# Optimization experiments

Measured on AMD Instinct MI355X. Metric: run time of the kernel, lower is better.

Reference implementation:

```python
import jax, jax.numpy as jnp
import numpy as np

N_HEAD = 16
D_HEAD = 64
D_MODEL = 1024
B, T = 2, 2048


def setup_inputs() -> dict:
    key = jax.random.key(0)
    ks = jax.random.split(key, 5)
    s = 1.0 / np.sqrt(D_MODEL)
    return {
        "x": jax.random.normal(ks[0], (B, T, D_MODEL), dtype=jnp.float32),
        "wq": jax.random.normal(ks[1], (D_MODEL, D_MODEL), dtype=jnp.float32) * s,
        "wk": jax.random.normal(ks[2], (D_MODEL, D_MODEL), dtype=jnp.float32) * s,
        "wv": jax.random.normal(ks[3], (D_MODEL, D_MODEL), dtype=jnp.float32) * s,
        "wo": jax.random.normal(ks[4], (D_MODEL, D_MODEL), dtype=jnp.float32) * s,
    }


def reference(x, wq, wk, wv, wo):
    Bb, Tt, D = x.shape
    H, Dh = N_HEAD, D_HEAD
    # Linear projections (flax Linear: y = x @ kernel), split heads
    q = (x @ wq).reshape(Bb, Tt, H, Dh)
    k = (x @ wk).reshape(Bb, Tt, H, Dh)
    v = (x @ wv).reshape(Bb, Tt, H, Dh)
    scale = jnp.sqrt(jnp.asarray(Dh)).astype(x.dtype)
    scores = jnp.einsum('bthd,bshd->bhts', q, k) / scale  # [B,H,T,T]
    mask = jnp.tril(jnp.ones((Tt, Tt), dtype=jnp.bool_))
    scores = jnp.where(mask, scores, jnp.finfo(scores.dtype).min)
    attn = jax.nn.softmax(scores, axis=-1)
    out = jnp.einsum('bhts,bshd->bthd', attn, v).reshape(Bb, Tt, D)
    return out @ wo
```

## Files before the change

kernel.cpp:

```cpp
#include <hip/hip_runtime.h>
#include <math.h>

#define DEV static __device__ __forceinline__

typedef __attribute__((ext_vector_type(4))) float f32x4;
typedef __attribute__((ext_vector_type(2))) unsigned u32x2;
typedef __attribute__((ext_vector_type(8))) __bf16 bf16x8;
typedef __attribute__((ext_vector_type(8))) unsigned short u16x8;
typedef __attribute__((ext_vector_type(4))) unsigned short u16x4;

constexpr int TB = 2;
constexpr int TT = 2048;
constexpr int DM = 1024;
constexpr int NH = 16;
constexpr int DH = 64;
constexpr int MR = TB * TT;
constexpr int SQKV = 3 * DM;

DEV unsigned short f2bf(float f) {
  union { float f; unsigned u; } v; v.f = f;
  return (unsigned short)((v.u + 0x7FFFu + ((v.u >> 16) & 1u)) >> 16);
}

DEV unsigned cvtpk(float a, float b) {
  unsigned r;
  asm("v_cvt_pk_bf16_f32 %0, %1, %2" : "=v"(r) : "v"(a), "v"(b));
  return r;
}

DEV void gld16(const void* g, void* l) {
  __builtin_amdgcn_global_load_lds((const __attribute__((address_space(1))) void*)g,
                                   (__attribute__((address_space(3))) void*)l, 16, 0, 0);
}

DEV bf16x8 ldsb8(const unsigned short* p) { return *(const bf16x8*)p; }

__global__ __launch_bounds__(256) void k_prep(const float* __restrict__ x,
                                              const float* __restrict__ w0,
                                              const float* __restrict__ w1,
                                              const float* __restrict__ w2,
                                              const float* __restrict__ w3,
                                              unsigned short* __restrict__ xb,
                                              unsigned short* __restrict__ wtdst) {
  __shared__ float tile[32][33];
  const int id = blockIdx.x, tid = threadIdx.x;
  if (id < 4096) {
    const int z = id >> 10, tl = id & 1023;
    const float* w = z == 0 ? w0 : z == 1 ? w1 : z == 2 ? w2 : w3;
    unsigned short* wt = wtdst + (size_t)z * DM * DM;
    const int n0 = (tl & 31) * 32, k0 = (tl >> 5) * 32;
    const int tx = tid & 31, ty = tid >> 5;
#pragma unroll
    for (int yy = 0; yy < 32; yy += 8)
      tile[ty + yy][tx] = w[(size_t)(k0 + ty + yy) * DM + n0 + tx];
    __syncthreads();
#pragma unroll
    for (int yy = 0; yy < 32; yy += 8)
      wt[(size_t)(n0 + ty + yy) * DM + k0 + tx] = f2bf(tile[tx][ty + yy]);
  } else {
    const int i = ((id - 4096) * 256 + tid) * 8;
    f32x4 a = *(const f32x4*)(x + i);
    f32x4 b = *(const f32x4*)(x + i + 4);
    u16x8 o;
#pragma unroll
    for (int j = 0; j < 4; ++j) { o[j] = f2bf(a[j]); o[j + 4] = f2bf(b[j]); }
    *(u16x8*)(xb + i) = o;
  }
}

__global__ __launch_bounds__(512) void k_gemm_qkv(const unsigned short* __restrict__ A,
                                                  const unsigned short* __restrict__ Bt,
                                                  unsigned short* __restrict__ Qb,
                                                  float ascale,
                                                  unsigned short* __restrict__ kp,
                                                  unsigned short* __restrict__ vt) {
  constexpr int K = DM, NS = K / 32;
  __shared__ alignas(16) unsigned short As[2][128 * 32];
  __shared__ alignas(16) unsigned short Bs[2][128 * 32];
  const int tid = threadIdx.x;
  const int m0 = blockIdx.y * 128, n0 = blockIdx.x * 128;
  const int lane = tid & 63, w = tid >> 6;
  const int lr = lane & 15, lg = lane >> 4;
  const int wm = w >> 2, wn = w & 3;
  const int srow = tid >> 2, scc = (tid & 3) ^ ((srow >> 1) & 3);
  const unsigned short* Ab = A + (size_t)(m0 + srow) * K + scc * 8;
  const unsigned short* Bb = Bt + (size_t)(n0 + srow) * K + scc * 8;
  auto stage = [&](int buf, int s) {
    gld16(Ab + s * 32, (void*)(As[buf] + tid * 8));
    gld16(Bb + s * 32, (void*)(Bs[buf] + tid * 8));
  };
  f32x4 acc[4][2] = {};
  stage(0, 0);
  for (int s = 0; s < NS; ++s) {
    const int buf = s & 1;
    asm volatile("s_waitcnt vmcnt(0)" ::: "memory");
    __builtin_amdgcn_s_barrier();
    if (s + 1 < NS) stage(buf ^ 1, s + 1);
    bf16x8 af[4], bfr[2];
#pragma unroll
    for (int i = 0; i < 4; ++i) {
      const int row = wm * 64 + i * 16 + lr;
      af[i] = ldsb8(As[buf] + row * 32 + ((lg ^ ((row >> 1) & 3)) * 8));
    }
#pragma unroll
    for (int j = 0; j < 2; ++j) {
      const int row = wn * 32 + j * 16 + lr;
      bfr[j] = ldsb8(Bs[buf] + row * 32 + ((lg ^ ((row >> 1) & 3)) * 8));
    }
    __builtin_amdgcn_s_setprio(1);
#pragma unroll
    for (int i = 0; i < 4; ++i)
#pragma unroll
      for (int j = 0; j < 2; ++j)
        acc[i][j] = __builtin_amdgcn_mfma_f32_16x16x32_bf16(af[i], bfr[j], acc[i][j], 0, 0, 0);
    __builtin_amdgcn_s_setprio(0);
  }
#pragma unroll
  for (int i = 0; i < 4; ++i)
#pragma unroll
    for (int j = 0; j < 2; ++j) {
      const int row = m0 + wm * 64 + i * 16 + lg * 4;
      const int col = n0 + wn * 32 + j * 16 + lr;
      const int bb = row >> 11, sg = row & (TT - 1);
      if (col < DM) {
#pragma unroll
        for (int r = 0; r < 4; ++r)
          Qb[(size_t)(row + r) * DM + col] = f2bf(acc[i][j][r] * ascale);
      } else if (col < 2 * DM) {
        const int hh = (col - DM) >> 6, dd = (col - DM) & 63;
        unsigned short* kb = kp + (size_t)(bb * NH + hh) * 32 * 4096;
#pragma unroll
        for (int r = 0; r < 4; ++r) {
          const int s = sg + r, t = s >> 6, sl = s & 63;
          kb[t * 4096 + sl * 64 + (((dd >> 3) ^ (sl & 7)) * 8) + (dd & 7)] = f2bf(acc[i][j][r]);
        }
      } else {
        const int hh = (col - 2 * DM) >> 6, dd = (col - 2 * DM) & 63;
        const int t = sg >> 6, sl = sg & 63;
        const int g = ((sl >> 5) << 2) | ((sl >> 2) & 3);
        const int hf2 = (sl >> 4) & 1;
        const int cch = g ^ (dd & 7);
        u16x4 pk;
#pragma unroll
        for (int r = 0; r < 4; ++r) pk[r] = f2bf(acc[i][j][r]);
        *(u16x4*)(vt + (size_t)((bb * NH + hh) * 32 + t) * 4096 + dd * 64 + cch * 8 + hf2 * 4) = pk;
      }
    }
}

__global__ __launch_bounds__(512) void k_gemm_out(const unsigned short* __restrict__ A,
                                                  const unsigned short* __restrict__ Bt,
                                                  float* __restrict__ C) {
  constexpr int K = DM, N = DM, NS = K / 32;
  __shared__ alignas(16) unsigned short As[2][128 * 32];
  __shared__ alignas(16) unsigned short Bs[2][64 * 32];
  const int tid = threadIdx.x;
  const int m0 = blockIdx.y * 128, n0 = blockIdx.x * 64;
  const int lane = tid & 63, w = tid >> 6;
  const int lr = lane & 15, lg = lane >> 4;
  const int wm = w >> 1, wn = w & 1;
  const int srow = tid >> 2, scc = (tid & 3) ^ ((srow >> 1) & 3);
  const unsigned short* Ab = A + (size_t)(m0 + srow) * K + scc * 8;
  const unsigned short* Bb = (tid < 256) ? Bt + (size_t)(n0 + srow) * K + scc * 8 : nullptr;
  auto stage = [&](int buf, int s) {
    gld16(Ab + s * 32, (void*)(As[buf] + tid * 8));
    if (tid < 256) gld16(Bb + s * 32, (void*)(Bs[buf] + tid * 8));
  };
  f32x4 acc[2][2] = {};
  stage(0, 0);
  for (int s = 0; s < NS; ++s) {
    const int buf = s & 1;
    asm volatile("s_waitcnt vmcnt(0)" ::: "memory");
    __builtin_amdgcn_s_barrier();
    if (s + 1 < NS) stage(buf ^ 1, s + 1);
    bf16x8 af[2], bfr[2];
#pragma unroll
    for (int i = 0; i < 2; ++i) {
      const int row = wm * 32 + i * 16 + lr;
      af[i] = ldsb8(As[buf] + row * 32 + ((lg ^ ((row >> 1) & 3)) * 8));
    }
#pragma unroll
    for (int j = 0; j < 2; ++j) {
      const int row = wn * 32 + j * 16 + lr;
      bfr[j] = ldsb8(Bs[buf] + row * 32 + ((lg ^ ((row >> 1) & 3)) * 8));
    }
    __builtin_amdgcn_s_setprio(1);
#pragma unroll
    for (int i = 0; i < 2; ++i)
#pragma unroll
      for (int j = 0; j < 2; ++j)
        acc[i][j] = __builtin_amdgcn_mfma_f32_16x16x32_bf16(af[i], bfr[j], acc[i][j], 0, 0, 0);
    __builtin_amdgcn_s_setprio(0);
  }
#pragma unroll
  for (int i = 0; i < 2; ++i)
#pragma unroll
    for (int j = 0; j < 2; ++j) {
      const int row = m0 + wm * 32 + i * 16 + lg * 4;
      const int col = n0 + wn * 32 + j * 16 + lr;
#pragma unroll
      for (int r = 0; r < 4; ++r) C[(size_t)(row + r) * N + col] = acc[i][j][r];
    }
}

__constant__ const signed char JV[24]  = {15,7,14,14,13,13,12,11, 15,6,12,10,10,9,11,5, 0,1,2,3,8,4,8,9};
__constant__ const signed char T0v[24] = {0,0,0,15,0,14,13,12, 16,0,0,0,11,0,0,0, 0,0,0,0,0,0,9,10};
__constant__ const signed char CNTv[24]= {16,16,15,15,14,14,13,12, 16,14,13,11,11,10,12,12, 2,4,6,8,9,10,9,10};

__global__ __launch_bounds__(512) void k_attn13(const unsigned short* __restrict__ Qb,
                                                const unsigned short* __restrict__ Kp,
                                                const unsigned short* __restrict__ Vt,
                                                unsigned short* __restrict__ O,
                                                float* __restrict__ Oacc0,
                                                float* __restrict__ Oacc1,
                                                float* __restrict__ lacc0,
                                                float* __restrict__ lacc1) {
  __shared__ alignas(16) unsigned short Ks[3][64 * 64];
  __shared__ alignas(16) unsigned short Vs[3][64 * 64];
  const int id = blockIdx.x;
  const int rank = id >> 5, bh = id & 31;
  const int j = JV[rank], t0 = T0v[rank], cnt = CNTv[rank];
  const bool split = (j >= 8);
  const int hf = (t0 > 0) ? 1 : 0;
  const int b = bh >> 4, h = bh & 15;
  const int q0 = j * 128;
  const int tid = threadIdx.x, lane = tid & 63, w = tid >> 6;
  const int lr = lane & 15, lg = lane >> 4;
  const int lsw = lr & 7;
  const int qw = q0 + w * 16;
  const unsigned short* Qg = Qb + (size_t)b * TT * DM + h * DH;
  const unsigned short* kbase = Kp + (size_t)bh * 32 * 4096 + tid * 8;
  const unsigned short* vbase = Vt + (size_t)bh * 32 * 4096 + tid * 8;

  bf16x8 qf[2];
#pragma unroll
  for (int c2 = 0; c2 < 2; ++c2)
    qf[c2] = *(const bf16x8*)(Qg + (size_t)(qw + lr) * DM + c2 * 32 + lg * 8);

  f32x4 acco[4] = {};
  float lrun = 0.f;

  auto stage = [&](int buf, int t) {
    gld16(kbase + (size_t)t * 4096, (void*)(Ks[buf] + tid * 8));
    gld16(vbase + (size_t)t * 4096, (void*)(Vs[buf] + tid * 8));
  };

  stage(0, t0);
  stage(1, t0 + 1);
  int buf = 0;
  for (int k = 0; k < cnt; ++k) {
    const int t = t0 + k;
    if (k + 1 < cnt) {
      asm volatile("s_waitcnt vmcnt(2)" ::: "memory");
    } else {
      asm volatile("s_waitcnt vmcnt(0)" ::: "memory");
    }
    __builtin_amdgcn_s_barrier();
    if (k + 2 < cnt) {
      int nb = buf + 2; if (nb >= 3) nb -= 3;
      stage(nb, t + 2);
    }
    const int s0 = t * 64;
    if (s0 <= qw + 15) {
      const unsigned short* Kb_ = Ks[buf];
      const unsigned short* Vb_ = Vs[buf];
      f32x4 st[4] = {};
      __builtin_amdgcn_s_setprio(1);
#pragma unroll
      for (int ct = 0; ct < 4; ++ct)
#pragma unroll
        for (int c2 = 0; c2 < 2; ++c2) {
          bf16x8 kf = ldsb8(Kb_ + (ct * 16 + lr) * 64 + (((c2 * 4 + lg) ^ lsw) * 8));
          st[ct] = __builtin_amdgcn_mfma_f32_16x16x32_bf16(kf, qf[c2], st[ct], 0, 0, 0);
        }
      __builtin_amdgcn_s_setprio(0);
      float p[4][4];
      const int qrel = qw + lr - s0;
      if (s0 + 63 >= qw) {
#pragma unroll
        for (int ct = 0; ct < 4; ++ct)
#pragma unroll
          for (int r = 0; r < 4; ++r) {
            float v = st[ct][r];
            if (ct * 16 + lg * 4 + r > qrel) v = -1e30f;
            p[ct][r] = v;
          }
      } else {
#pragma unroll
        for (int ct = 0; ct < 4; ++ct)
#pragma unroll
          for (int r = 0; r < 4; ++r) p[ct][r] = st[ct][r];
      }
      f32x4 rs4 = {0.f, 0.f, 0.f, 0.f};
#pragma unroll
      for (int ct = 0; ct < 4; ++ct)
#pragma unroll
        for (int r = 0; r < 4; ++r) {
          p[ct][r] = __builtin_exp2f(p[ct][r]);
          rs4[r] += p[ct][r];
        }
      float rs = (rs4[0] + rs4[1]) + (rs4[2] + rs4[3]);
      rs += __shfl_xor(rs, 16);
      rs += __shfl_xor(rs, 32);
      lrun += rs;
      bf16x8 pf[2];
#pragma unroll
      for (int ks = 0; ks < 2; ++ks) {
        union { unsigned w4[4]; bf16x8 v; } pu;
        pu.w4[0] = cvtpk(p[2 * ks][0], p[2 * ks][1]);
        pu.w4[1] = cvtpk(p[2 * ks][2], p[2 * ks][3]);
        pu.w4[2] = cvtpk(p[2 * ks + 1][0], p[2 * ks + 1][1]);
        pu.w4[3] = cvtpk(p[2 * ks + 1][2], p[2 * ks + 1][3]);
        pf[ks] = pu.v;
      }
      __builtin_amdgcn_s_setprio(1);
#pragma unroll
      for (int dt = 0; dt < 4; ++dt) {
        const unsigned short* Vrow = Vb_ + (dt * 16 + lr) * 64;
#pragma unroll
        for (int ks = 0; ks < 2; ++ks) {
          bf16x8 vf = ldsb8(Vrow + (((ks * 4 + lg) ^ lsw) * 8));
          acco[dt] = __builtin_amdgcn_mfma_f32_16x16x32_bf16(pf[ks], vf, acco[dt], 0, 0, 0);
        }
      }
      __builtin_amdgcn_s_setprio(0);
    }
    if (++buf >= 3) buf = 0;
  }
  if (!split) {
    const float linv = 1.f / lrun;
    float lb[4];
#pragma unroll
    for (int r = 0; r < 4; ++r) lb[r] = __shfl(linv, lg * 4 + r);
#pragma unroll
    for (int dt = 0; dt < 4; ++dt)
#pragma unroll
      for (int r = 0; r < 4; ++r) {
        const int q = qw + lg * 4 + r;
        O[(size_t)(b * TT + q) * DM + h * DH + dt * 16 + lr] = f2bf(acco[dt][r] * lb[r]);
      }
  } else {
    const int jj = j - 8;
    float* Oa = (hf ? Oacc1 : Oacc0) + (size_t)(bh * 8 + jj) * 128 * 64;
    float* la = (hf ? lacc1 : lacc0) + (size_t)(bh * 8 + jj) * 128;
#pragma unroll
    for (int dt = 0; dt < 4; ++dt)
#pragma unroll
      for (int r = 0; r < 4; ++r)
        Oa[(w * 16 + lg * 4 + r) * 64 + dt * 16 + lr] = acco[dt][r];
    if (lg == 0) la[w * 16 + lr] = lrun;
  }
}

__global__ __launch_bounds__(256) void k_norm(const float* __restrict__ Oacc0,
                                              const float* __restrict__ Oacc1,
                                              const float* __restrict__ lacc0,
                                              const float* __restrict__ lacc1,
                                              unsigned short* __restrict__ O) {
  const int gid = blockIdx.x * 256 + threadIdx.x;
  const int f = gid * 8;
  const int d0 = f & 63, row = (f >> 6) & 127, jj = (f >> 13) & 7, bh = f >> 16;
  const int b = bh >> 4, h = bh & 15;
  const size_t ri = (size_t)(bh * 8 + jj) * 128 + row;
  const size_t oi = ri * 64 + d0;
  f32x4 a0 = *(const f32x4*)(Oacc0 + oi);
  f32x4 a1 = *(const f32x4*)(Oacc0 + oi + 4);
  f32x4 b0 = *(const f32x4*)(Oacc1 + oi);
  f32x4 b1 = *(const f32x4*)(Oacc1 + oi + 4);
  const float linv = 1.f / (lacc0[ri] + lacc1[ri]);
  u16x8 o;
#pragma unroll
  for (int r = 0; r < 4; ++r) {
    o[r] = f2bf((a0[r] + b0[r]) * linv);
    o[r + 4] = f2bf((a1[r] + b1[r]) * linv);
  }
  const int q = 1024 + jj * 128 + row;
  *(u16x8*)(O + (size_t)(b * TT + q) * DM + h * DH + d0) = o;
}

extern "C" void kernel_launch(void* const* d_in, const int* in_sizes, int n_in,
                              void* d_out, int out_size, void* d_ws, size_t ws_size,
                              hipStream_t stream) {
  const float* x = (const float*)d_in[0];
  const float* wq = (const float*)d_in[1];
  const float* wk = (const float*)d_in[2];
  const float* wv = (const float*)d_in[3];
  const float* wo = (const float*)d_in[4];
  float* out = (float*)d_out;
  char* ws = (char*)d_ws;
  const size_t MB = 1u << 20;
  unsigned short* xb = (unsigned short*)(ws);
  float* Oacc0 = (float*)(ws);
  unsigned short* wqt = (unsigned short*)(ws + 8 * MB);
  float* lacc0 = (float*)(ws + 8 * MB);
  float* lacc1 = (float*)(ws + 8 * MB + (32 * 8 * 128) * 4);
  unsigned short* wot = (unsigned short*)(ws + 14 * MB);
  unsigned short* Qb = (unsigned short*)(ws + 16 * MB);
  unsigned short* Kp = (unsigned short*)(ws + 24 * MB);
  unsigned short* Vtb = (unsigned short*)(ws + 32 * MB);
  float* Oacc1 = (float*)(ws + 40 * MB);

  k_prep<<<dim3(6144), 256, 0, stream>>>(x, wq, wk, wv, wo, xb, wqt);
  k_gemm_qkv<<<dim3(24, 32), 512, 0, stream>>>(xb, wqt, Qb, 0.18033688f, Kp, Vtb);
  k_attn13<<<dim3(768), 512, 0, stream>>>(Qb, Kp, Vtb, Qb, Oacc0, Oacc1, lacc0, lacc1);
  k_norm<<<dim3(1024), 256, 0, stream>>>(Oacc0, Oacc1, lacc0, lacc1, Qb);
  k_gemm_out<<<dim3(16, 32), 512, 0, stream>>>(Qb, wot, out);
}
```

Measured before the change: 106.4 us.

## Software-pipeline attention loop: overlap next QK^T with previous PV MFMA

Restructures the attention inner loop so that each iteration computes QK^T for the current tile, then does the PV MFMA for the previous tile's probabilities, then softmax/exp for the current tile. This interleaves MFMA work with exp/convert VALU work across iterations to hide latency. K now uses two LDS buffers and V three, with staggered prefetch and a drain step after the loop. It also drops the no-sync staging of two tiles ahead, so global-load latency hiding is shallower.

```diff
diff --git a/kernel.cpp b/kernel.cpp
--- a/kernel.cpp
+++ b/kernel.cpp
@@ -207,7 +207,7 @@
 __constant__ const signed char T0v[24] = {0,0,0,15,0,14,13,12, 16,0,0,0,11,0,0,0, 0,0,0,0,0,0,9,10};
 __constant__ const signed char CNTv[24]= {16,16,15,15,14,14,13,12, 16,14,13,11,11,10,12,12, 2,4,6,8,9,10,9,10};
 
-__global__ __launch_bounds__(512) void k_attn13(const unsigned short* __restrict__ Qb,
+__global__ __launch_bounds__(512) void k_attn14(const unsigned short* __restrict__ Qb,
                                                 const unsigned short* __restrict__ Kp,
                                                 const unsigned short* __restrict__ Vt,
                                                 unsigned short* __restrict__ O,
@@ -215,7 +215,7 @@
                                                 float* __restrict__ Oacc1,
                                                 float* __restrict__ lacc0,
                                                 float* __restrict__ lacc1) {
-  __shared__ alignas(16) unsigned short Ks[3][64 * 64];
+  __shared__ alignas(16) unsigned short Ks[2][64 * 64];
   __shared__ alignas(16) unsigned short Vs[3][64 * 64];
   const int id = blockIdx.x;
   const int rank = id >> 5, bh = id & 31;
@@ -240,31 +240,24 @@
   f32x4 acco[4] = {};
   float lrun = 0.f;
 
-  auto stage = [&](int buf, int t) {
-    gld16(kbase + (size_t)t * 4096, (void*)(Ks[buf] + tid * 8));
-    gld16(vbase + (size_t)t * 4096, (void*)(Vs[buf] + tid * 8));
-  };
-
-  stage(0, t0);
-  stage(1, t0 + 1);
-  int buf = 0;
+  auto stageK = [&](int t) { gld16(kbase + (size_t)t * 4096, (void*)(Ks[t & 1] + tid * 8)); };
+  auto stageV = [&](int t) { gld16(vbase + (size_t)t * 4096, (void*)(Vs[t % 3] + tid * 8)); };
+
+  stageK(t0);
+  stageV(t0);
+  bf16x8 pfP[2];
+  bool actPrev = false;
+  int tPrev = 0;
   for (int k = 0; k < cnt; ++k) {
     const int t = t0 + k;
-    if (k + 1 < cnt) {
-      asm volatile("s_waitcnt vmcnt(2)" ::: "memory");
-    } else {
-      asm volatile("s_waitcnt vmcnt(0)" ::: "memory");
-    }
+    asm volatile("s_waitcnt vmcnt(1)" ::: "memory");
     __builtin_amdgcn_s_barrier();
-    if (k + 2 < cnt) {
-      int nb = buf + 2; if (nb >= 3) nb -= 3;
-      stage(nb, t + 2);
-    }
+    if (k + 1 < cnt) stageK(t + 1);
     const int s0 = t * 64;
-    if (s0 <= qw + 15) {
-      const unsigned short* Kb_ = Ks[buf];
-      const unsigned short* Vb_ = Vs[buf];
-      f32x4 st[4] = {};
+    const bool act = (s0 <= qw + 15);
+    f32x4 st[4] = {};
+    if (act) {
+      const unsigned short* Kb_ = Ks[t & 1];
       __builtin_amdgcn_s_setprio(1);
 #pragma unroll
       for (int ct = 0; ct < 4; ++ct)
@@ -274,6 +267,22 @@
           st[ct] = __builtin_amdgcn_mfma_f32_16x16x32_bf16(kf, qf[c2], st[ct], 0, 0, 0);
         }
       __builtin_amdgcn_s_setprio(0);
+    }
+    if (actPrev) {
+      const unsigned short* Vb_ = Vs[tPrev % 3];
+      __builtin_amdgcn_s_setprio(1);
+#pragma unroll
+      for (int dt = 0; dt < 4; ++dt) {
+        const unsigned short* Vrow = Vb_ + (dt * 16 + lr) * 64;
+#pragma unroll
+        for (int ks = 0; ks < 2; ++ks) {
+          bf16x8 vf = ldsb8(Vrow + (((ks * 4 + lg) ^ lsw) * 8));
+          acco[dt] = __builtin_amdgcn_mfma_f32_16x16x32_bf16(pfP[ks], vf, acco[dt], 0, 0, 0);
+        }
+      }
+      __builtin_amdgcn_s_setprio(0);
+    }
+    if (act) {
       float p[4][4];
       const int qrel = qw + lr - s0;
       if (s0 + 63 >= qw) {
@@ -303,7 +312,6 @@
       rs += __shfl_xor(rs, 16);
       rs += __shfl_xor(rs, 32);
       lrun += rs;
-      bf16x8 pf[2];
 #pragma unroll
       for (int ks = 0; ks < 2; ++ks) {
         union { unsigned w4[4]; bf16x8 v; } pu;
@@ -311,21 +319,26 @@
         pu.w4[1] = cvtpk(p[2 * ks][2], p[2 * ks][3]);
         pu.w4[2] = cvtpk(p[2 * ks + 1][0], p[2 * ks + 1][1]);
         pu.w4[3] = cvtpk(p[2 * ks + 1][2], p[2 * ks + 1][3]);
-        pf[ks] = pu.v;
-      }
-      __builtin_amdgcn_s_setprio(1);
-#pragma unroll
-      for (int dt = 0; dt < 4; ++dt) {
-        const unsigned short* Vrow = Vb_ + (dt * 16 + lr) * 64;
-#pragma unroll
-        for (int ks = 0; ks < 2; ++ks) {
-          bf16x8 vf = ldsb8(Vrow + (((ks * 4 + lg) ^ lsw) * 8));
-          acco[dt] = __builtin_amdgcn_mfma_f32_16x16x32_bf16(pf[ks], vf, acco[dt], 0, 0, 0);
-        }
-      }
-      __builtin_amdgcn_s_setprio(0);
-    }
-    if (++buf >= 3) buf = 0;
+        pfP[ks] = pu.v;
+      }
+    }
+    if (k + 1 < cnt) stageV(t + 1);
+    actPrev = act;
+    tPrev = t;
+  }
+  asm volatile("s_waitcnt vmcnt(0)" ::: "memory");
+  __builtin_amdgcn_s_barrier();
+  if (actPrev) {
+    const unsigned short* Vb_ = Vs[tPrev % 3];
+#pragma unroll
+    for (int dt = 0; dt < 4; ++dt) {
+      const unsigned short* Vrow = Vb_ + (dt * 16 + lr) * 64;
+#pragma unroll
+      for (int ks = 0; ks < 2; ++ks) {
+        bf16x8 vf = ldsb8(Vrow + (((ks * 4 + lg) ^ lsw) * 8));
+        acco[dt] = __builtin_amdgcn_mfma_f32_16x16x32_bf16(pfP[ks], vf, acco[dt], 0, 0, 0);
+      }
+    }
   }
   if (!split) {
     const float linv = 1.f / lrun;
@@ -402,7 +415,7 @@
 
   k_prep<<<dim3(6144), 256, 0, stream>>>(x, wq, wk, wv, wo, xb, wqt);
   k_gemm_qkv<<<dim3(24, 32), 512, 0, stream>>>(xb, wqt, Qb, 0.18033688f, Kp, Vtb);
-  k_attn13<<<dim3(768), 512, 0, stream>>>(Qb, Kp, Vtb, Qb, Oacc0, Oacc1, lacc0, lacc1);
+  k_attn14<<<dim3(768), 512, 0, stream>>>(Qb, Kp, Vtb, Qb, Oacc0, Oacc1, lacc0, lacc1);
   k_norm<<<dim3(1024), 256, 0, stream>>>(Oacc0, Oacc1, lacc0, lacc1, Qb);
   k_gemm_out<<<dim3(16, 32), 512, 0, stream>>>(Qb, wot, out);
 }
```

Result: slower. 116.1 us (+9.1%).
